# Kernel tuning notes

Hardware: AMD Instinct MI355X
Metric: run time of the kernel (lower is better)

## Reference

```python
import jax, jax.numpy as jnp
import numpy as np

NUM_HEADS = 16
DIM_HEAD = 64
HIDDEN = 1024
CONTEXT = 200
MAX_POS = 512
INNER = NUM_HEADS * DIM_HEAD


def setup_inputs() -> dict:
    key = jax.random.key(0)
    ks = jax.random.split(key, 8)
    B, T = 8, 4000  # T is a multiple of CONTEXT (remainder == 0)
    s = 0.02
    return {
        "hidden_states": jax.random.normal(ks[0], (B, T, HIDDEN), jnp.float32),
        "ln_w": jnp.ones((HIDDEN,), jnp.float32),
        "ln_b": jnp.zeros((HIDDEN,), jnp.float32),
        "wq": jax.random.normal(ks[1], (HIDDEN, INNER), jnp.float32) * s,
        "wkv": jax.random.normal(ks[2], (HIDDEN, 2 * INNER), jnp.float32) * s,
        "wo": jax.random.normal(ks[3], (INNER, HIDDEN), jnp.float32) * s,
        "bo": jnp.zeros((HIDDEN,), jnp.float32),
        "rel_emb": jax.random.normal(ks[4], (2 * MAX_POS + 1, DIM_HEAD), jnp.float32) * s,
    }


def reference(hidden_states, ln_w, ln_b, wq, wkv, wo, bo, rel_emb):
    B, T, _ = hidden_states.shape
    nb = T // CONTEXT  # remainder == 0 by construction
    scale = DIM_HEAD ** -0.5

    # pre-norm (LayerNorm, eps=1e-5)
    mu = jnp.mean(hidden_states, axis=-1, keepdims=True)
    var = jnp.mean(jnp.square(hidden_states - mu), axis=-1, keepdims=True)
    x = (hidden_states - mu) * jax.lax.rsqrt(var + 1e-5) * ln_w + ln_b

    q = x @ wq                       # (B, T, INNER)
    kv = x @ wkv                     # (B, T, 2*INNER)
    k, v = jnp.split(kv, 2, axis=-1)

    def blk(t):  # (B, T, INNER) -> (B, nb, H, C, D)
        return t.reshape(B, nb, CONTEXT, NUM_HEADS, DIM_HEAD).transpose(0, 1, 3, 2, 4)

    q, k, v = blk(q), blk(k), blk(v)

    # Shaw relative position embeddings within a block
    seq = jnp.arange(CONTEXT)
    dist = jnp.clip(seq[:, None] - seq[None, :], -CONTEXT, CONTEXT) + MAX_POS
    rel = rel_emb[dist]              # (C, C, D)

    # pos bias: sum over head dim of q * rel  (einsum instead of broadcast-multiply-sum)
    pos_attn = jnp.einsum('bnhid,ijd->bnhij', q, rel) * scale

    # SDPA math path: softmax(q k^T * scale + bias) v
    scores = jnp.einsum('bnhid,bnhjd->bnhij', q, k) * scale + pos_attn
    attn = jax.nn.softmax(scores, axis=-1)
    out = jnp.einsum('bnhij,bnhjd->bnhid', attn, v)  # (B, nb, H, C, D)

    out = out.transpose(0, 1, 3, 2, 4).reshape(B, T, INNER)
    return out @ wo + bo  # dropout is identity in eval
```

## Files before the change

kernel.cpp:

```cpp
#include <hip/hip_runtime.h>
#include <stdint.h>
#include <stddef.h>

#define NTOK   32000
#define HID    1024
#define NQKV   3072
#define CTX    200
#define NH     16

typedef _Float16 f16;
typedef _Float16 f16x8 __attribute__((ext_vector_type(8)));
typedef _Float16 f16x4 __attribute__((ext_vector_type(4)));
typedef float    f32x4 __attribute__((ext_vector_type(4)));

__device__ __forceinline__ void async_copy16(const void* g, void* l) {
  typedef const __attribute__((address_space(1))) char gchar;
  typedef __attribute__((address_space(3))) char lchar;
  __builtin_amdgcn_global_load_lds((gchar*)g, (lchar*)l, 16, 0, 0);
}

__global__ __launch_bounds__(256) void prep_kernel(
    const float* __restrict__ wq, const float* __restrict__ wkv,
    const float* __restrict__ wo, const float* __restrict__ rel,
    f16* __restrict__ wt_qkv, f16* __restrict__ wt_o, f16* __restrict__ rel_h) {
  long idx = (long)blockIdx.x * 256 + threadIdx.x;
  if (idx < (long)NQKV * HID) {
    int n = (int)(idx >> 10), k = (int)(idx & 1023);
    float v = (n < 1024) ? wq[(size_t)k * 1024 + n] : wkv[(size_t)k * 2048 + (n - 1024)];
    wt_qkv[idx] = (f16)v;
    return;
  }
  idx -= (long)NQKV * HID;
  if (idx < (long)HID * HID) {
    int n = (int)(idx >> 10), k = (int)(idx & 1023);
    wt_o[idx] = (f16)wo[(size_t)k * 1024 + n];
    return;
  }
  idx -= (long)HID * HID;
  if (idx < 1025 * 64) rel_h[idx] = (f16)rel[idx];
}

__global__ __launch_bounds__(256) void ln_kernel(
    const float* __restrict__ hs, const float* __restrict__ lw,
    const float* __restrict__ lb, f16* __restrict__ x) {
  int tok = blockIdx.x;
  int t = threadIdx.x;
  const float4* src = (const float4*)(hs + (size_t)tok * HID);
  float4 v = src[t];
  float s  = v.x + v.y + v.z + v.w;
  float s2 = v.x * v.x + v.y * v.y + v.z * v.z + v.w * v.w;
  for (int m = 1; m < 64; m <<= 1) { s += __shfl_xor(s, m); s2 += __shfl_xor(s2, m); }
  __shared__ float ps[4], ps2[4];
  int w = t >> 6;
  if ((t & 63) == 0) { ps[w] = s; ps2[w] = s2; }
  __syncthreads();
  s  = ps[0] + ps[1] + ps[2] + ps[3];
  s2 = ps2[0] + ps2[1] + ps2[2] + ps2[3];
  float mu  = s * (1.0f / 1024.0f);
  float var = s2 * (1.0f / 1024.0f) - mu * mu;
  float rs  = rsqrtf(var + 1e-5f);
  float4 wv = ((const float4*)lw)[t];
  float4 bv = ((const float4*)lb)[t];
  f16x4 o;
  o[0] = (f16)((v.x - mu) * rs * wv.x + bv.x);
  o[1] = (f16)((v.y - mu) * rs * wv.y + bv.y);
  o[2] = (f16)((v.z - mu) * rs * wv.z + bv.z);
  o[3] = (f16)((v.w - mu) * rs * wv.w + bv.w);
  *(f16x4*)(x + (size_t)tok * HID + t * 4) = o;
}

template <int EPI>
__global__ __launch_bounds__(512, 2) void gemm_kernel(
    const f16* __restrict__ A, const f16* __restrict__ Bt,
    void* __restrict__ C, const float* __restrict__ bias, int N) {
  __shared__ __attribute__((aligned(16))) f16 sm[4][16384];

  int t = threadIdx.x;
  int w = t >> 6, l = t & 63;
  int wm = w >> 2, wn = w & 3;
  int lr = l & 15, lk = l >> 4;
  int sw = lr & 7;
  const int sg_off = ((l >> 3) << 10) + (((l & 7) ^ (l >> 3)) << 3);

  int nwg = (int)(gridDim.x * gridDim.y);
  int lid = (int)(blockIdx.y * gridDim.x + blockIdx.x);
  int q = nwg >> 3, r = nwg & 7;
  int xcd = lid & 7, loc = lid >> 3;
  int nid = (xcd < r ? xcd * (q + 1) : r * (q + 1) + (xcd - r) * q) + loc;
  int bx = nid % (int)gridDim.x, by = nid / (int)gridDim.x;
  const int m0 = by * 256, n0 = bx * 256;

  f32x4 acc[8][4] = {};
  f16x8 a[8], b[8];

#define STG(reg, half, gsrc, row0, kt) do {                                        \
    const f16* _s = (gsrc) + (size_t)((row0) + (half) * 128 + w * 16) * 1024       \
                    + (kt) * 64 + sg_off;                                          \
    char* _d = (char*)(reg) + (half) * 16384 + w * 2048;                           \
    async_copy16(_s, _d);                                                          \
    async_copy16(_s + 8 * 1024, _d + 1024);                                        \
  } while (0)

#define LDA(As_, Mh) do {                                                          \
    _Pragma("unroll") for (int mt = 0; mt < 4; ++mt) {                             \
      int row_ = wm * 128 + (Mh) * 64 + mt * 16 + lr;                              \
      _Pragma("unroll") for (int ks = 0; ks < 2; ++ks)                             \
        a[mt * 2 + ks] = *(const f16x8*)((As_) + row_ * 64                         \
                          + (((ks * 4 + lk) ^ sw) << 3));                          \
    } } while (0)

#define LDB(Bs_, Nh) do {                                                          \
    _Pragma("unroll") for (int nt = 0; nt < 2; ++nt) {                             \
      int row_ = wn * 64 + (Nh) * 32 + nt * 16 + lr;                               \
      _Pragma("unroll") for (int ks = 0; ks < 2; ++ks)                             \
        b[(Nh) * 4 + nt * 2 + ks] = *(const f16x8*)((Bs_) + row_ * 64              \
                          + (((ks * 4 + lk) ^ sw) << 3));                          \
    } } while (0)

#define MMA(Mh, Nh) do {                                                           \
    __builtin_amdgcn_s_setprio(1);                                                 \
    _Pragma("unroll") for (int mt = 0; mt < 4; ++mt)                               \
    _Pragma("unroll") for (int nt = 0; nt < 2; ++nt)                               \
    _Pragma("unroll") for (int ks = 0; ks < 2; ++ks)                               \
      acc[(Mh) * 4 + mt][(Nh) * 2 + nt] = __builtin_amdgcn_mfma_f32_16x16x32_f16(  \
          a[mt * 2 + ks], b[(Nh) * 4 + nt * 2 + ks],                               \
          acc[(Mh) * 4 + mt][(Nh) * 2 + nt], 0, 0, 0);                             \
    __builtin_amdgcn_s_setprio(0); } while (0)

#define BAR  __builtin_amdgcn_s_barrier()
#define WLG  asm volatile("s_waitcnt lgkmcnt(0)" ::: "memory")
#define WVM6 asm volatile("s_waitcnt vmcnt(6)" ::: "memory")

  STG(sm[1], 0, Bt, n0, 0);
  STG(sm[1], 1, Bt, n0, 0);
  STG(sm[0], 0, A, m0, 0);
  STG(sm[0], 1, A, m0, 0);
  asm volatile("s_waitcnt vmcnt(4)" ::: "memory");
  STG(sm[3], 0, Bt, n0, 1);
  STG(sm[3], 1, Bt, n0, 1);
  STG(sm[2], 0, A, m0, 1);
  WVM6;
  BAR;

  for (int j = 0; j < 8; ++j) {
    int k1 = 2 * j + 1;
    int ke = (2 * j + 2 > 14) ? 14 : 2 * j + 2;
    int ko = (2 * j + 3 > 15) ? 15 : 2 * j + 3;
    LDA(sm[0], 0); LDB(sm[1], 0);
    STG(sm[2], 1, A, m0, k1);
    BAR; WLG; MMA(0, 0); BAR;
    LDB(sm[1], 1);
    STG(sm[1], 0, Bt, n0, ke);
    BAR; WLG; MMA(0, 1); BAR;
    LDA(sm[0], 1);
    STG(sm[1], 1, Bt, n0, ke);
    BAR; WLG; MMA(1, 0); BAR;
    STG(sm[0], 0, A, m0, ke);
    BAR; MMA(1, 1); WVM6; BAR;
    LDA(sm[2], 0); LDB(sm[3], 0);
    STG(sm[0], 1, A, m0, ke);
    BAR; WLG; MMA(0, 0); BAR;
    LDB(sm[3], 1);
    STG(sm[3], 0, Bt, n0, ko);
    BAR; WLG; MMA(0, 1); BAR;
    LDA(sm[2], 1);
    STG(sm[3], 1, Bt, n0, ko);
    BAR; WLG; MMA(1, 0); BAR;
    STG(sm[2], 0, A, m0, ko);
    BAR; MMA(1, 1); WVM6; BAR;
  }

#undef STG
#undef LDA
#undef LDB
#undef MMA
#undef BAR
#undef WLG
#undef WVM6

  if constexpr (EPI == 0) {
    #pragma unroll
    for (int mt = 0; mt < 8; ++mt) {
      #pragma unroll
      for (int rr = 0; rr < 4; ++rr) {
        int grow = m0 + wm * 128 + mt * 16 + lk * 4 + rr;
        unsigned bn = (unsigned)grow / 200u;
        unsigned io = (unsigned)grow - bn * 200u;
        size_t rowb = (size_t)bn * 614400 + (size_t)io * 64;
        #pragma unroll
        for (int nt = 0; nt < 4; ++nt) {
          int gcol = n0 + wn * 64 + nt * 16 + lr;
          int sel = gcol >> 10;
          int hh  = (gcol >> 6) & 15;
          int d   = gcol & 63;
          ((f16*)C)[rowb + (size_t)(hh * 3 + sel) * 12800 + d] = (f16)acc[mt][nt][rr];
        }
      }
    }
  } else {
    #pragma unroll
    for (int mt = 0; mt < 8; ++mt)
      #pragma unroll
      for (int nt = 0; nt < 4; ++nt) {
        int gcol = n0 + wn * 64 + nt * 16 + lr;
        float bv = bias[gcol];
        #pragma unroll
        for (int rr = 0; rr < 4; ++rr) {
          int grow = m0 + wm * 128 + mt * 16 + lk * 4 + rr;
          ((float*)C)[(size_t)grow * N + gcol] = acc[mt][nt][rr] + bv;
        }
      }
  }
}

__global__ __launch_bounds__(256, 2) void attn_kernel(
    const f16* __restrict__ qkvb, const f16* __restrict__ rel_h,
    f16* __restrict__ out) {
  __shared__ __attribute__((aligned(16))) f16 Ks[208 * 64];
  __shared__ __attribute__((aligned(16))) f16 Vt[64 * 200];
  __shared__ __attribute__((aligned(16))) f16 Gb[4][215 * 17];

  int bh = blockIdx.x;
  int h  = bh & 15;
  size_t t0 = (size_t)(bh >> 4) * CTX;
  int t = threadIdx.x;
  int w = t >> 6, l = t & 63;
  int lr = l & 15, lk = l >> 4;

  const f16* Qb = qkvb + (size_t)bh * 38400;
  const f16* Kb = Qb + 12800;
  const f16* Vb = Qb + 25600;

  for (int it = w; it < 26; it += 4) {
    int srow = it * 8 + (l >> 3);
    int pg   = l & 7;
    int grow = srow < 200 ? srow : 199;
    int gg   = pg ^ (srow & 7);
    async_copy16(Kb + (size_t)grow * 64 + gg * 8, (char*)Ks + it * 1024);
  }
  {
    const f16* vcol = Vb + l;
    for (int g = w; g < 50; g += 4) {
      int j = g * 4;
      f16x4 pk;
      #pragma unroll
      for (int u = 0; u < 4; ++u) pk[u] = vcol[(size_t)(j + u) * 64];
      *(f16x4*)(Vt + l * 200 + j) = pk;
    }
  }
  __syncthreads();

  f16* gb = Gb[w];

  for (int c = w; c < 13; c += 4) {
    int m0 = c * 16;
    int qrow = m0 + lr; if (qrow > 199) qrow = 199;
    f16x8 bq0 = *(const f16x8*)(Qb + (size_t)qrow * 64 + lk * 8);
    f16x8 bq1 = *(const f16x8*)(Qb + (size_t)qrow * 64 + 32 + lk * 8);
    bq0 = bq0 * (f16)0.125f;
    bq1 = bq1 * (f16)0.125f;

    f32x4 S[13];
    #pragma unroll
    for (int ts = 0; ts < 13; ++ts) {
      int row = ts * 16 + lr;
      int sw  = row & 7;
      f16x8 a0 = *(const f16x8*)(Ks + row * 64 + (lk ^ sw) * 8);
      f16x8 a1 = *(const f16x8*)(Ks + row * 64 + ((4 + lk) ^ sw) * 8);
      f32x4 a = {};
      a = __builtin_amdgcn_mfma_f32_16x16x32_f16(a0, bq0, a, 0, 0, 0);
      S[ts] = __builtin_amdgcn_mfma_f32_16x16x32_f16(a1, bq1, a, 0, 0, 0);
    }

    const f16* rb = rel_h + (size_t)(313 + m0) * 64;
    #pragma unroll
    for (int tg = 0; tg < 14; ++tg) {
      int pr = tg * 16 + lr;
      f16x8 a0 = *(const f16x8*)(rb + (size_t)pr * 64 + lk * 8);
      f16x8 a1 = *(const f16x8*)(rb + (size_t)pr * 64 + 32 + lk * 8);
      f32x4 g = {};
      g = __builtin_amdgcn_mfma_f32_16x16x32_f16(a0, bq0, g, 0, 0, 0);
      g = __builtin_amdgcn_mfma_f32_16x16x32_f16(a1, bq1, g, 0, 0, 0);
      #pragma unroll
      for (int r = 0; r < 4; ++r) {
        int pp2 = tg * 16 + 4 * lk + r;
        if (pp2 <= 214) gb[pp2 * 17 + lr] = (f16)g[r];
      }
    }

    #pragma unroll
    for (int ts = 0; ts < 13; ++ts) {
      #pragma unroll
      for (int r = 0; r < 4; ++r) {
        int pp = lr + 199 - ts * 16 - 4 * lk - r;
        if (pp < 0) pp = 0;
        S[ts][r] += (float)gb[pp * 17 + lr];
      }
    }
    #pragma unroll
    for (int r = 0; r < 4; ++r)
      if (4 * lk + r >= 8) S[12][r] = -1e30f;

    float mx = -1e30f;
    #pragma unroll
    for (int ts = 0; ts < 13; ++ts)
      #pragma unroll
      for (int r = 0; r < 4; ++r) mx = fmaxf(mx, S[ts][r]);
    mx = fmaxf(mx, __shfl_xor(mx, 16));
    mx = fmaxf(mx, __shfl_xor(mx, 32));
    float sum = 0.f;
    #pragma unroll
    for (int ts = 0; ts < 13; ++ts)
      #pragma unroll
      for (int r = 0; r < 4; ++r) {
        float e = __expf(S[ts][r] - mx);
        S[ts][r] = e;
        sum += e;
      }
    sum += __shfl_xor(sum, 16);
    sum += __shfl_xor(sum, 32);
    float inv = 1.0f / sum;

    f16x4 P[13];
    #pragma unroll
    for (int ts = 0; ts < 13; ++ts)
      #pragma unroll
      for (int r = 0; r < 4; ++r) P[ts][r] = (f16)(S[ts][r] * inv);

    f32x4 o[4] = {};
    #pragma unroll
    for (int ts = 0; ts < 13; ++ts) {
      int col4 = ts * 16 + 4 * lk;
      if (col4 > 196) col4 = 196;
      #pragma unroll
      for (int dt = 0; dt < 4; ++dt) {
        f16x4 bv = *(const f16x4*)(Vt + (dt * 16 + lr) * 200 + col4);
        o[dt] = __builtin_amdgcn_mfma_f32_16x16x16f16(P[ts], bv, o[dt], 0, 0, 0);
      }
    }

    {
      f16* ob = gb;
      #pragma unroll
      for (int dt = 0; dt < 4; ++dt)
        #pragma unroll
        for (int r = 0; r < 4; ++r)
          ob[(4 * lk + r) * 72 + dt * 16 + lr] = (f16)o[dt][r];
      int orow = l >> 2;
      int ocol = (l & 3) * 16;
      if (m0 + orow < 200) {
        f16x8 v0 = *(const f16x8*)(ob + orow * 72 + ocol);
        f16x8 v1 = *(const f16x8*)(ob + orow * 72 + ocol + 8);
        f16* dst = out + (t0 + m0 + orow) * HID + h * 64 + ocol;
        *(f16x8*)dst = v0;
        *(f16x8*)(dst + 8) = v1;
      }
    }
  }
}

extern "C" void kernel_launch(void* const* d_in, const int* in_sizes, int n_in,
                              void* d_out, int out_size, void* d_ws, size_t ws_size,
                              hipStream_t stream) {
  const float* hs  = (const float*)d_in[0];
  const float* lnw = (const float*)d_in[1];
  const float* lnb = (const float*)d_in[2];
  const float* wq  = (const float*)d_in[3];
  const float* wkv = (const float*)d_in[4];
  const float* wo  = (const float*)d_in[5];
  const float* bo  = (const float*)d_in[6];
  const float* rel = (const float*)d_in[7];

  char* ws = (char*)d_ws;
  f16* x     = (f16*)(ws);
  f16* qkvb  = (f16*)(ws + 65536000);
  f16* wtqkv = (f16*)(ws + 65536000 + 196608000);
  f16* wto   = (f16*)(ws + 65536000 + 196608000 + 6291456);
  f16* rel_h = (f16*)(ws + 65536000 + 196608000 + 6291456 + 2097152);
  f16* attn  = x;

  {
    long total = (long)NQKV * HID + (long)HID * HID + 1025 * 64;
    int grid = (int)((total + 255) / 256);
    prep_kernel<<<grid, 256, 0, stream>>>(wq, wkv, wo, rel, wtqkv, wto, rel_h);
  }
  ln_kernel<<<NTOK, 256, 0, stream>>>(hs, lnw, lnb, x);
  gemm_kernel<0><<<dim3(NQKV / 256, NTOK / 256), 512, 0, stream>>>(x, wtqkv, (void*)qkvb, nullptr, NQKV);
  attn_kernel<<<2560, 256, 0, stream>>>(qkvb, rel_h, attn);
  gemm_kernel<1><<<dim3(HID / 256, NTOK / 256), 512, 0, stream>>>(attn, wto, d_out, bo, HID);
}
```

Baseline: 682.9 us.

## Stage GEMM epilogues through LDS and read K directly in attention

The GEMM epilogues now stage accumulator tiles through LDS and write them out as 16-byte vectors. This replaces scattered scalar f16/f32 stores, and the addressing is simplified with precomputed base pointers and swizzle offsets. The attention kernel drops the K shared-memory staging and loads K fragments straight from global memory. It also transposes the rel-position scratch layout and raises occupancy to 3 blocks per CU. The risks are uncached global K loads repeated across waves and extra LDS round trips in the epilogue.

```diff
diff --git a/kernel.cpp b/kernel.cpp
--- a/kernel.cpp
+++ b/kernel.cpp
@@ -93,28 +93,33 @@
   f32x4 acc[8][4] = {};
   f16x8 a[8], b[8];
 
-#define STG(reg, half, gsrc, row0, kt) do {                                        \
-    const f16* _s = (gsrc) + (size_t)((row0) + (half) * 128 + w * 16) * 1024       \
-                    + (kt) * 64 + sg_off;                                          \
-    char* _d = (char*)(reg) + (half) * 16384 + w * 2048;                           \
+  const f16* a_src = A + (size_t)(m0 + w * 16) * 1024 + sg_off;
+  const f16* b_src = Bt + (size_t)(n0 + w * 16) * 1024 + sg_off;
+  char* lds_w = (char*)sm + w * 2048;
+  const int xo0 = (lk ^ sw) << 4;
+  const int xo1 = ((4 + lk) ^ sw) << 4;
+  const char* As_base = (const char*)sm + ((wm * 128 + lr) << 7);
+  const char* Bs_base = (const char*)sm + 32768 + ((wn * 64 + lr) << 7);
+
+#define STG(bufofs, half, src, kt) do {                                            \
+    const f16* _s = (src) + (half) * 131072 + (size_t)(kt) * 64;                   \
+    char* _d = lds_w + (bufofs) + (half) * 16384;                                  \
     async_copy16(_s, _d);                                                          \
-    async_copy16(_s + 8 * 1024, _d + 1024);                                        \
+    async_copy16(_s + 8192, _d + 1024);                                            \
   } while (0)
 
-#define LDA(As_, Mh) do {                                                          \
+#define LDA(bo, Mh) do {                                                           \
     _Pragma("unroll") for (int mt = 0; mt < 4; ++mt) {                             \
-      int row_ = wm * 128 + (Mh) * 64 + mt * 16 + lr;                              \
-      _Pragma("unroll") for (int ks = 0; ks < 2; ++ks)                             \
-        a[mt * 2 + ks] = *(const f16x8*)((As_) + row_ * 64                         \
-                          + (((ks * 4 + lk) ^ sw) << 3));                          \
+      const char* _p = As_base + (bo) + (((Mh) * 64 + mt * 16) << 7);              \
+      a[mt * 2 + 0] = *(const f16x8*)(_p + xo0);                                   \
+      a[mt * 2 + 1] = *(const f16x8*)(_p + xo1);                                   \
     } } while (0)
 
-#define LDB(Bs_, Nh) do {                                                          \
+#define LDB(bo, Nh) do {                                                           \
     _Pragma("unroll") for (int nt = 0; nt < 2; ++nt) {                             \
-      int row_ = wn * 64 + (Nh) * 32 + nt * 16 + lr;                               \
-      _Pragma("unroll") for (int ks = 0; ks < 2; ++ks)                             \
-        b[(Nh) * 4 + nt * 2 + ks] = *(const f16x8*)((Bs_) + row_ * 64              \
-                          + (((ks * 4 + lk) ^ sw) << 3));                          \
+      const char* _p = Bs_base + (bo) + (((Nh) * 32 + nt * 16) << 7);              \
+      b[(Nh) * 4 + nt * 2 + 0] = *(const f16x8*)(_p + xo0);                        \
+      b[(Nh) * 4 + nt * 2 + 1] = *(const f16x8*)(_p + xo1);                        \
     } } while (0)
 
 #define MMA(Mh, Nh) do {                                                           \
@@ -131,14 +136,14 @@
 #define WLG  asm volatile("s_waitcnt lgkmcnt(0)" ::: "memory")
 #define WVM6 asm volatile("s_waitcnt vmcnt(6)" ::: "memory")
 
-  STG(sm[1], 0, Bt, n0, 0);
-  STG(sm[1], 1, Bt, n0, 0);
-  STG(sm[0], 0, A, m0, 0);
-  STG(sm[0], 1, A, m0, 0);
+  STG(32768, 0, b_src, 0);
+  STG(32768, 1, b_src, 0);
+  STG(0,     0, a_src, 0);
+  STG(0,     1, a_src, 0);
   asm volatile("s_waitcnt vmcnt(4)" ::: "memory");
-  STG(sm[3], 0, Bt, n0, 1);
-  STG(sm[3], 1, Bt, n0, 1);
-  STG(sm[2], 0, A, m0, 1);
+  STG(98304, 0, b_src, 1);
+  STG(98304, 1, b_src, 1);
+  STG(65536, 0, a_src, 1);
   WVM6;
   BAR;
 
@@ -146,27 +151,27 @@
     int k1 = 2 * j + 1;
     int ke = (2 * j + 2 > 14) ? 14 : 2 * j + 2;
     int ko = (2 * j + 3 > 15) ? 15 : 2 * j + 3;
-    LDA(sm[0], 0); LDB(sm[1], 0);
-    STG(sm[2], 1, A, m0, k1);
+    LDA(0, 0); LDB(0, 0);
+    STG(65536, 1, a_src, k1);
     BAR; WLG; MMA(0, 0); BAR;
-    LDB(sm[1], 1);
-    STG(sm[1], 0, Bt, n0, ke);
+    LDB(0, 1);
+    STG(32768, 0, b_src, ke);
     BAR; WLG; MMA(0, 1); BAR;
-    LDA(sm[0], 1);
-    STG(sm[1], 1, Bt, n0, ke);
+    LDA(0, 1);
+    STG(32768, 1, b_src, ke);
     BAR; WLG; MMA(1, 0); BAR;
-    STG(sm[0], 0, A, m0, ke);
+    STG(0, 0, a_src, ke);
     BAR; MMA(1, 1); WVM6; BAR;
-    LDA(sm[2], 0); LDB(sm[3], 0);
-    STG(sm[0], 1, A, m0, ke);
+    LDA(65536, 0); LDB(65536, 0);
+    STG(0, 1, a_src, ke);
     BAR; WLG; MMA(0, 0); BAR;
-    LDB(sm[3], 1);
-    STG(sm[3], 0, Bt, n0, ko);
+    LDB(65536, 1);
+    STG(98304, 0, b_src, ko);
     BAR; WLG; MMA(0, 1); BAR;
-    LDA(sm[2], 1);
-    STG(sm[3], 1, Bt, n0, ko);
+    LDA(65536, 1);
+    STG(98304, 1, b_src, ko);
     BAR; WLG; MMA(1, 0); BAR;
-    STG(sm[2], 0, A, m0, ko);
+    STG(65536, 0, a_src, ko);
     BAR; MMA(1, 1); WVM6; BAR;
   }
 
@@ -178,47 +183,62 @@
 #undef WLG
 #undef WVM6
 
+  asm volatile("s_waitcnt vmcnt(0)" ::: "memory");
+  __builtin_amdgcn_s_barrier();
+
   if constexpr (EPI == 0) {
+    f16* scr = (f16*)sm + (size_t)w * 1152;
+    int gcb = n0 + wn * 64;
+    int sel = gcb >> 10;
+    int hh  = (gcb >> 6) & 15;
+    f16* cb = (f16*)C + (size_t)(hh * 3 + sel) * 12800;
+    int orow = l >> 2;
+    int ocol = (l & 3) * 16;
+    int cbase = ocol ^ ((orow & 8) << 1);
     #pragma unroll
     for (int mt = 0; mt < 8; ++mt) {
       #pragma unroll
-      for (int rr = 0; rr < 4; ++rr) {
-        int grow = m0 + wm * 128 + mt * 16 + lk * 4 + rr;
-        unsigned bn = (unsigned)grow / 200u;
-        unsigned io = (unsigned)grow - bn * 200u;
-        size_t rowb = (size_t)bn * 614400 + (size_t)io * 64;
+      for (int nt = 0; nt < 4; ++nt)
         #pragma unroll
-        for (int nt = 0; nt < 4; ++nt) {
-          int gcol = n0 + wn * 64 + nt * 16 + lr;
-          int sel = gcol >> 10;
-          int hh  = (gcol >> 6) & 15;
-          int d   = gcol & 63;
-          ((f16*)C)[rowb + (size_t)(hh * 3 + sel) * 12800 + d] = (f16)acc[mt][nt][rr];
-        }
-      }
+        for (int rr = 0; rr < 4; ++rr)
+          scr[(lk * 4 + rr) * 72 + ((nt * 16 + lr) ^ ((lk & 2) << 3))] = (f16)acc[mt][nt][rr];
+      int grow = m0 + wm * 128 + mt * 16 + orow;
+      unsigned bn = (unsigned)grow / 200u;
+      unsigned io = (unsigned)grow - bn * 200u;
+      f16x8 v0 = *(const f16x8*)(scr + orow * 72 + cbase);
+      f16x8 v1 = *(const f16x8*)(scr + orow * 72 + cbase + 8);
+      f16* dst = cb + (size_t)bn * 614400 + (size_t)io * 64 + ocol;
+      *(f16x8*)dst = v0;
+      *(f16x8*)(dst + 8) = v1;
     }
   } else {
-    #pragma unroll
-    for (int mt = 0; mt < 8; ++mt)
-      #pragma unroll
-      for (int nt = 0; nt < 4; ++nt) {
-        int gcol = n0 + wn * 64 + nt * 16 + lr;
-        float bv = bias[gcol];
+    float* scr = (float*)sm + (size_t)w * 1088;
+    float bv[4];
+    #pragma unroll
+    for (int nt = 0; nt < 4; ++nt) bv[nt] = bias[n0 + wn * 64 + nt * 16 + lr];
+    int orow = l >> 2;
+    int ocol = (l & 3) * 16;
+    #pragma unroll
+    for (int mt = 0; mt < 8; ++mt) {
+      #pragma unroll
+      for (int nt = 0; nt < 4; ++nt)
         #pragma unroll
-        for (int rr = 0; rr < 4; ++rr) {
-          int grow = m0 + wm * 128 + mt * 16 + lk * 4 + rr;
-          ((float*)C)[(size_t)grow * N + gcol] = acc[mt][nt][rr] + bv;
-        }
-      }
-  }
-}
-
-__global__ __launch_bounds__(256, 2) void attn_kernel(
+        for (int rr = 0; rr < 4; ++rr)
+          scr[(lk * 4 + rr) * 68 + nt * 16 + lr] = acc[mt][nt][rr] + bv[nt];
+      int grow = m0 + wm * 128 + mt * 16 + orow;
+      float* dst = (float*)C + (size_t)grow * N + n0 + wn * 64 + ocol;
+      #pragma unroll
+      for (int i = 0; i < 4; ++i)
+        *(float4*)(dst + i * 4) = *(const float4*)(scr + orow * 68 + ocol + i * 4);
+    }
+  }
+}
+
+__global__ __launch_bounds__(256, 3) void attn_kernel(
     const f16* __restrict__ qkvb, const f16* __restrict__ rel_h,
     f16* __restrict__ out) {
-  __shared__ __attribute__((aligned(16))) f16 Ks[208 * 64];
   __shared__ __attribute__((aligned(16))) f16 Vt[64 * 200];
-  __shared__ __attribute__((aligned(16))) f16 Gb[4][215 * 17];
+  __shared__ __attribute__((aligned(16))) f16 Gt[4][16 * 225];
 
   int bh = blockIdx.x;
   int h  = bh & 15;
@@ -231,13 +251,6 @@
   const f16* Kb = Qb + 12800;
   const f16* Vb = Qb + 25600;
 
-  for (int it = w; it < 26; it += 4) {
-    int srow = it * 8 + (l >> 3);
-    int pg   = l & 7;
-    int grow = srow < 200 ? srow : 199;
-    int gg   = pg ^ (srow & 7);
-    async_copy16(Kb + (size_t)grow * 64 + gg * 8, (char*)Ks + it * 1024);
-  }
   {
     const f16* vcol = Vb + l;
     for (int g = w; g < 50; g += 4) {
@@ -250,7 +263,11 @@
   }
   __syncthreads();
 
-  f16* gb = Gb[w];
+  f16* gt = Gt[w];
+  const int lr225 = lr * 225;
+  const int wofs  = lr225 + 4 * lk;
+  const int gofs  = lr * 226 - 4 * lk;
+  const f16* kb_l = Kb + lr * 64 + lk * 8;
 
   for (int c = w; c < 13; c += 4) {
     int m0 = c * 16;
@@ -263,28 +280,27 @@
     f32x4 S[13];
     #pragma unroll
     for (int ts = 0; ts < 13; ++ts) {
-      int row = ts * 16 + lr;
-      int sw  = row & 7;
-      f16x8 a0 = *(const f16x8*)(Ks + row * 64 + (lk ^ sw) * 8);
-      f16x8 a1 = *(const f16x8*)(Ks + row * 64 + ((4 + lk) ^ sw) * 8);
-      f32x4 a = {};
-      a = __builtin_amdgcn_mfma_f32_16x16x32_f16(a0, bq0, a, 0, 0, 0);
-      S[ts] = __builtin_amdgcn_mfma_f32_16x16x32_f16(a1, bq1, a, 0, 0, 0);
-    }
-
-    const f16* rb = rel_h + (size_t)(313 + m0) * 64;
+      const f16* ka = kb_l + ts * 1024;
+      if (ts == 12 && lr >= 8) ka = Kb + 199 * 64 + lk * 8;
+      f16x8 a0 = *(const f16x8*)(ka);
+      f16x8 a1 = *(const f16x8*)(ka + 32);
+      f32x4 s0 = {};
+      s0 = __builtin_amdgcn_mfma_f32_16x16x32_f16(a0, bq0, s0, 0, 0, 0);
+      S[ts] = __builtin_amdgcn_mfma_f32_16x16x32_f16(a1, bq1, s0, 0, 0, 0);
+    }
+
+    const f16* rb = rel_h + (size_t)(313 + m0) * 64 + lr * 64 + lk * 8;
     #pragma unroll
     for (int tg = 0; tg < 14; ++tg) {
-      int pr = tg * 16 + lr;
-      f16x8 a0 = *(const f16x8*)(rb + (size_t)pr * 64 + lk * 8);
-      f16x8 a1 = *(const f16x8*)(rb + (size_t)pr * 64 + 32 + lk * 8);
+      f16x8 a0 = *(const f16x8*)(rb + tg * 1024);
+      f16x8 a1 = *(const f16x8*)(rb + tg * 1024 + 32);
       f32x4 g = {};
       g = __builtin_amdgcn_mfma_f32_16x16x32_f16(a0, bq0, g, 0, 0, 0);
       g = __builtin_amdgcn_mfma_f32_16x16x32_f16(a1, bq1, g, 0, 0, 0);
       #pragma unroll
       for (int r = 0; r < 4; ++r) {
-        int pp2 = tg * 16 + 4 * lk + r;
-        if (pp2 <= 214) gb[pp2 * 17 + lr] = (f16)g[r];
+        if (tg < 13 || 4 * lk + r <= 6)
+          gt[wofs + 16 * tg + r] = (f16)g[r];
       }
     }
 
@@ -292,9 +308,9 @@
     for (int ts = 0; ts < 13; ++ts) {
       #pragma unroll
       for (int r = 0; r < 4; ++r) {
-        int pp = lr + 199 - ts * 16 - 4 * lk - r;
-        if (pp < 0) pp = 0;
-        S[ts][r] += (float)gb[pp * 17 + lr];
+        int idx = gofs + 199 - ts * 16 - r;
+        if (ts == 12 && idx < lr225) idx = lr225;
+        S[ts][r] += (float)gt[idx];
       }
     }
     #pragma unroll
@@ -340,7 +356,7 @@
     }
 
     {
-      f16* ob = gb;
+      f16* ob = gt;
       #pragma unroll
       for (int dt = 0; dt < 4; ++dt)
         #pragma unroll
```

Result: slower. 886.2 us (+29.8%).
